# Performance work log

Hardware: AMD Instinct MI355X
Metric: run time of the kernel (lower is better)

Reference implementation:

```python
import jax, jax.numpy as jnp
import numpy as np

N = 100000       # nodes
E = 1600000      # edges (before self-loops)
IN_DIM = 64
HIDDEN = 32
HEADS = 2
OUT_DIM = 32
NEG_SLOPE = 0.2  # PyG GATConv default leaky_relu slope


def setup_inputs() -> dict:
    key = jax.random.key(0)
    ks = jax.random.split(key, 10)
    x = jax.random.normal(ks[0], (N, IN_DIM), dtype=jnp.float32)
    edge_index = jax.random.randint(ks[1], (2, E), 0, N, dtype=jnp.int64)
    s = 0.1
    W1 = jax.random.normal(ks[2], (IN_DIM, HEADS * HIDDEN), dtype=jnp.float32) * s
    a1_src = jax.random.normal(ks[3], (HEADS, HIDDEN), dtype=jnp.float32) * s
    a1_dst = jax.random.normal(ks[4], (HEADS, HIDDEN), dtype=jnp.float32) * s
    b1 = jnp.zeros((HEADS * HIDDEN,), dtype=jnp.float32)
    W2 = jax.random.normal(ks[5], (HEADS * HIDDEN, OUT_DIM), dtype=jnp.float32) * s
    a2_src = jax.random.normal(ks[6], (1, OUT_DIM), dtype=jnp.float32) * s
    a2_dst = jax.random.normal(ks[7], (1, OUT_DIM), dtype=jnp.float32) * s
    b2 = jnp.zeros((OUT_DIM,), dtype=jnp.float32)
    return {"x": x, "edge_index": edge_index,
            "W1": W1, "a1_src": a1_src, "a1_dst": a1_dst, "b1": b1,
            "W2": W2, "a2_src": a2_src, "a2_dst": a2_dst, "b2": b2}


def _gat_layer(x, src, dst, W, a_src, a_dst, bias, heads, d, concat):
    n = x.shape[0]
    # per-head linear transform: [n, heads, d]
    h = (x @ W).reshape(n, heads, d)
    # per-node attention logit halves: [n, heads]
    alpha_s = jnp.einsum('nhd,hd->nh', h, a_src)
    alpha_d = jnp.einsum('nhd,hd->nh', h, a_dst)
    # edge logits + leaky_relu: [e, heads]
    e = alpha_s[src] + alpha_d[dst]
    e = jnp.where(e >= 0, e, NEG_SLOPE * e)
    # numerically stable segment softmax over edges sharing a destination
    m = jax.ops.segment_max(e, dst, num_segments=n)          # [n, heads]
    p = jnp.exp(e - m[dst])                                  # [e, heads]
    z = jax.ops.segment_sum(p, dst, num_segments=n)          # [n, heads]
    alpha = p / z[dst]                                       # [e, heads]
    # weighted scatter-sum of source messages: [n, heads, d]
    out = jax.ops.segment_sum(alpha[:, :, None] * h[src], dst, num_segments=n)
    out = out.reshape(n, heads * d) if concat else out.mean(axis=1)
    return out + bias


def reference(x, edge_index, W1, a1_src, a1_dst, b1, W2, a2_src, a2_dst, b2):
    n = x.shape[0]
    # PyG GATConv default: add self-loops (guarantees nonempty softmax segments)
    loops = jnp.arange(n, dtype=edge_index.dtype)
    src = jnp.concatenate([edge_index[0], loops])
    dst = jnp.concatenate([edge_index[1], loops])
    h = _gat_layer(x, src, dst, W1, a1_src, a1_dst, b1, HEADS, HIDDEN, True)
    h = jax.nn.elu(h)
    # F.dropout(p=0.2) is identity at inference
    out = _gat_layer(h, src, dst, W2, a2_src, a2_dst, b2, 1, OUT_DIM, False)
    return out
```

## Files before the change

### kernel.cpp

```cpp
#include <hip/hip_runtime.h>
#include <math.h>

#define N_NODES 100000
#define E_EDGES 1600000
#define EA (E_EDGES + N_NODES)
#define NEG_SLOPE 0.2f
#define LG_BUCKET 8
#define BUCKET (1 << LG_BUCKET)
#define NB ((N_NODES + BUCKET - 1) >> LG_BUCKET)
#define LG_SLOTS 13
#define SLOTS (1 << LG_SLOTS)
#define CH 8192
#define NPB ((EA + CH - 1) / CH)
#define NLIN1 (N_NODES / 16)
#define SRC_BITS 17
#define SRC_MASK ((1u << SRC_BITS) - 1)
#define CAP 96

typedef _Float16 f16;
typedef _Float16 half2v __attribute__((ext_vector_type(2)));

__device__ __forceinline__ float leaky(float e) { return e >= 0.f ? e : NEG_SLOPE * e; }
__device__ __forceinline__ unsigned h2u(half2v h) { return __builtin_bit_cast(unsigned, h); }
__device__ __forceinline__ half2v u2h(unsigned u) { return __builtin_bit_cast(half2v, u); }
__device__ __forceinline__ half2v cvtpk(float a, float b) {
    return __builtin_bit_cast(half2v, __builtin_amdgcn_cvt_pkrtz(a, b));
}


__global__ __launch_bounds__(256) void part_lin1_kernel(
        const int* __restrict__ src, const int* __restrict__ dst,
        int* __restrict__ bcnt, unsigned* __restrict__ edges,
        const float* __restrict__ x, const float* __restrict__ W1,
        const float* __restrict__ a1s, const float* __restrict__ a1d,
        f16* __restrict__ h1, float* __restrict__ as1, float* __restrict__ ad1) {
    __shared__ int hist[NB];
    __shared__ int base[NB];
    __shared__ float Wl[64 * 64];
    __shared__ float xs[16 * 64];
    int t = threadIdx.x;
    if (blockIdx.x < NPB) {
        for (int i = t; i < NB; i += 256) hist[i] = 0;
        __syncthreads();
        int e0 = blockIdx.x * CH;
        int e1 = e0 + CH < EA ? e0 + CH : EA;
        for (int e = e0 + t; e < e1; e += 256) {
            int d = (e < E_EDGES) ? dst[e] : (e - E_EDGES);
            atomicAdd(&hist[d >> LG_BUCKET], 1);
        }
        __syncthreads();
        for (int i = t; i < NB; i += 256) {
            int h = hist[i];
            base[i] = h ? atomicAdd(&bcnt[i], h) : 0;
            hist[i] = 0;
        }
        __syncthreads();
        for (int e = e0 + t; e < e1; e += 256) {
            int s, d;
            if (e < E_EDGES) { s = src[e]; d = dst[e]; } else { s = e - E_EDGES; d = s; }
            int b = d >> LG_BUCKET;
            int r = base[b] + atomicAdd(&hist[b], 1);
            if (r < SLOTS)
                edges[(b << LG_SLOTS) + r] = ((unsigned)(d & (BUCKET - 1)) << SRC_BITS) | (unsigned)s;
        }
    } else {
        int r0 = (blockIdx.x - NPB) * 16;
        const float4* W4 = (const float4*)W1;
        float4* Wl4 = (float4*)Wl;
        #pragma unroll
        for (int i = 0; i < 4; i++) Wl4[t + i * 256] = W4[t + i * 256];
        ((float4*)xs)[t] = ((const float4*)(x + (size_t)r0 * 64))[t];
        __syncthreads();
        int c = t & 63, tg = t >> 6;
        float acc0 = 0.f, acc1 = 0.f, acc2 = 0.f, acc3 = 0.f;
        #pragma unroll
        for (int k = 0; k < 64; k++) {
            float w = Wl[k * 64 + c];
            acc0 += xs[(tg * 4 + 0) * 64 + k] * w;
            acc1 += xs[(tg * 4 + 1) * 64 + k] * w;
            acc2 += xs[(tg * 4 + 2) * 64 + k] * w;
            acc3 += xs[(tg * 4 + 3) * 64 + k] * w;
        }
        int r = r0 + tg * 4;
        h1[(size_t)(r + 0) * 64 + c] = (f16)acc0;
        h1[(size_t)(r + 1) * 64 + c] = (f16)acc1;
        h1[(size_t)(r + 2) * 64 + c] = (f16)acc2;
        h1[(size_t)(r + 3) * 64 + c] = (f16)acc3;
        float s_c = a1s[c], d_c = a1d[c];
        float vs0 = acc0 * s_c, vd0 = acc0 * d_c;
        float vs1 = acc1 * s_c, vd1 = acc1 * d_c;
        float vs2 = acc2 * s_c, vd2 = acc2 * d_c;
        float vs3 = acc3 * s_c, vd3 = acc3 * d_c;
        #pragma unroll
        for (int off = 16; off > 0; off >>= 1) {
            vs0 += __shfl_xor(vs0, off); vd0 += __shfl_xor(vd0, off);
            vs1 += __shfl_xor(vs1, off); vd1 += __shfl_xor(vd1, off);
            vs2 += __shfl_xor(vs2, off); vd2 += __shfl_xor(vd2, off);
            vs3 += __shfl_xor(vs3, off); vd3 += __shfl_xor(vd3, off);
        }
        if ((c & 31) == 0) {
            int h = c >> 5;
            as1[(r + 0) * 2 + h] = vs0; ad1[(r + 0) * 2 + h] = vd0;
            as1[(r + 1) * 2 + h] = vs1; ad1[(r + 1) * 2 + h] = vd1;
            as1[(r + 2) * 2 + h] = vs2; ad1[(r + 2) * 2 + h] = vd2;
            as1[(r + 3) * 2 + h] = vs3; ad1[(r + 3) * 2 + h] = vd3;
        }
    }
}

__global__ __launch_bounds__(256) void bucket_scatter(unsigned* __restrict__ edges,
                                                      const int* __restrict__ bcnt,
                                                      int2* __restrict__ rowSD) {
    __shared__ unsigned stage[SLOTS];
    __shared__ int hist[256];
    __shared__ int sc[256];
    int b = blockIdx.x;
    int t = threadIdx.x;
    int node0 = b << LG_BUCKET;
    int cnt = bcnt[b]; if (cnt > SLOTS) cnt = SLOTS;
    int baseg = b << LG_SLOTS;
    hist[t] = 0;
    __syncthreads();
    for (int i = t; i < cnt; i += 256) {
        unsigned p = edges[baseg + i];
        stage[i] = p;
        atomicAdd(&hist[p >> SRC_BITS], 1);
    }
    __syncthreads();
    int v = hist[t];
    sc[t] = v;
    __syncthreads();
    for (int off = 1; off < 256; off <<= 1) {
        int x = (t >= off) ? sc[t - off] : 0;
        __syncthreads();
        sc[t] += x;
        __syncthreads();
    }
    int excl = sc[t] - v;
    if (t < BUCKET && node0 + t < N_NODES) rowSD[node0 + t] = make_int2(baseg + excl, v);
    hist[t] = excl;
    __syncthreads();
    for (int i = t; i < cnt; i += 256) {
        unsigned p = stage[i];
        int r = atomicAdd(&hist[p >> SRC_BITS], 1);
        edges[baseg + r] = p & SRC_MASK;
    }
}


__global__ __launch_bounds__(256) void agg1_kernel(
        const int2* __restrict__ rowSD, const int* __restrict__ srcs,
        const f16* __restrict__ h1, const float* __restrict__ as1,
        const float* __restrict__ ad1, const float* __restrict__ b1,
        const float* __restrict__ W2, const float* __restrict__ a2s,
        const float* __restrict__ a2d,
        f16* __restrict__ h2, float* __restrict__ as2, float* __restrict__ ad2) {
    __shared__ float rowb[32][68];
    __shared__ float W2l[64 * 32];
    int tid = threadIdx.x;
    for (int i = tid; i < 2048; i += 256) W2l[i] = W2[i];
    int owid = tid >> 3;
    int l = tid & 7;
    int hh = l >> 2;
    int v = blockIdx.x * 32 + owid;
    int2 sd = rowSD[v];
    int start = sd.x, deg = sd.y;
    float2 adv = ((const float2*)ad1)[v];
    const float2* as1v2 = (const float2*)as1;
    const uint4* h1q = (const uint4*)h1;
    unsigned psel = hh ? 0x03020302u : 0x01000100u;
    half2v ax0 = {}, ax1 = {}, ax2 = {}, ax3 = {};
    half2v bx0 = {}, bx1 = {}, bx2 = {}, bx3 = {};
    float z0 = 0.f, z1 = 0.f;
    for (int c = 0; c < deg; c += 8) {
        int cnt = deg - c; if (cnt > 8) cnt = 8;
        int sreg = 0, pki = 0;
        if (c + l < deg) {
            sreg = srcs[start + c + l];
            float2 a = as1v2[sreg];
            half2v pk = cvtpk(__expf(leaky(a.x + adv.x)), __expf(leaky(a.y + adv.y)));
            z0 += (float)pk.x;
            z1 += (float)pk.y;
            pki = (int)h2u(pk);
        }
        int j = 0;
        for (; j + 1 < cnt; j += 2) {
            int s0 = __shfl(sreg, j, 8), s1 = __shfl(sreg, j + 1, 8);
            unsigned u0 = (unsigned)__shfl(pki, j, 8);
            unsigned u1 = (unsigned)__shfl(pki, j + 1, 8);
            uint4 g0 = h1q[(size_t)s0 * 8 + l];
            uint4 g1 = h1q[(size_t)s1 * 8 + l];
            half2v p0 = u2h(__builtin_amdgcn_perm(u0, u0, psel));
            half2v p1 = u2h(__builtin_amdgcn_perm(u1, u1, psel));
            ax0 += p0 * u2h(g0.x); ax1 += p0 * u2h(g0.y);
            ax2 += p0 * u2h(g0.z); ax3 += p0 * u2h(g0.w);
            bx0 += p1 * u2h(g1.x); bx1 += p1 * u2h(g1.y);
            bx2 += p1 * u2h(g1.z); bx3 += p1 * u2h(g1.w);
        }
        if (j < cnt) {
            int s0 = __shfl(sreg, j, 8);
            unsigned u0 = (unsigned)__shfl(pki, j, 8);
            uint4 g0 = h1q[(size_t)s0 * 8 + l];
            half2v p0 = u2h(__builtin_amdgcn_perm(u0, u0, psel));
            ax0 += p0 * u2h(g0.x); ax1 += p0 * u2h(g0.y);
            ax2 += p0 * u2h(g0.z); ax3 += p0 * u2h(g0.w);
        }
    }
    #pragma unroll
    for (int off = 4; off > 0; off >>= 1) {
        z0 += __shfl_xor(z0, off);
        z1 += __shfl_xor(z1, off);
    }
    float rz = 1.f / (hh ? z1 : z0);
    half2v t0 = ax0 + bx0, t1 = ax1 + bx1, t2 = ax2 + bx2, t3 = ax3 + bx3;
    float4 ba = ((const float4*)b1)[2 * l];
    float4 bb = ((const float4*)b1)[2 * l + 1];
    float o0 = (float)t0.x * rz + ba.x;
    float o1 = (float)t0.y * rz + ba.y;
    float o2 = (float)t1.x * rz + ba.z;
    float o3 = (float)t1.y * rz + ba.w;
    float o4 = (float)t2.x * rz + bb.x;
    float o5 = (float)t2.y * rz + bb.y;
    float o6 = (float)t3.x * rz + bb.z;
    float o7 = (float)t3.y * rz + bb.w;
    o0 = o0 > 0.f ? o0 : __expf(o0) - 1.f;
    o1 = o1 > 0.f ? o1 : __expf(o1) - 1.f;
    o2 = o2 > 0.f ? o2 : __expf(o2) - 1.f;
    o3 = o3 > 0.f ? o3 : __expf(o3) - 1.f;
    o4 = o4 > 0.f ? o4 : __expf(o4) - 1.f;
    o5 = o5 > 0.f ? o5 : __expf(o5) - 1.f;
    o6 = o6 > 0.f ? o6 : __expf(o6) - 1.f;
    o7 = o7 > 0.f ? o7 : __expf(o7) - 1.f;
    rowb[owid][8 * l]     = o0;
    rowb[owid][8 * l + 1] = o1;
    rowb[owid][8 * l + 2] = o2;
    rowb[owid][8 * l + 3] = o3;
    rowb[owid][8 * l + 4] = o4;
    rowb[owid][8 * l + 5] = o5;
    rowb[owid][8 * l + 6] = o6;
    rowb[owid][8 * l + 7] = o7;
    __syncthreads();
    float hc0 = 0.f, hc1 = 0.f, hc2 = 0.f, hc3 = 0.f;
    #pragma unroll 8
    for (int k = 0; k < 64; k++) {
        float r = rowb[owid][k];
        hc0 += r * W2l[k * 32 + 4 * l];
        hc1 += r * W2l[k * 32 + 4 * l + 1];
        hc2 += r * W2l[k * 32 + 4 * l + 2];
        hc3 += r * W2l[k * 32 + 4 * l + 3];
    }
    half2v hlo, hhi;
    hlo.x = (f16)hc0; hlo.y = (f16)hc1;
    hhi.x = (f16)hc2; hhi.y = (f16)hc3;
    uint2 hw; hw.x = h2u(hlo); hw.y = h2u(hhi);
    ((uint2*)h2)[(size_t)v * 8 + l] = hw;
    float4 sa = ((const float4*)a2s)[l];
    float4 da = ((const float4*)a2d)[l];
    float vs = hc0 * sa.x + hc1 * sa.y + hc2 * sa.z + hc3 * sa.w;
    float vd = hc0 * da.x + hc1 * da.y + hc2 * da.z + hc3 * da.w;
    #pragma unroll
    for (int off = 4; off > 0; off >>= 1) { vs += __shfl_xor(vs, off); vd += __shfl_xor(vd, off); }
    if (l == 0) { as2[v] = vs; ad2[v] = vd; }
}


__global__ __launch_bounds__(256) void agg2_kernel(
        const int2* __restrict__ rowSD, const int* __restrict__ srcs,
        const f16* __restrict__ h2, const float* __restrict__ as2,
        const float* __restrict__ ad2, const float* __restrict__ b2,
        float* __restrict__ out) {
    __shared__ float pbuf2[4][CAP];
    int wid = threadIdx.x >> 6;
    int v = blockIdx.x * 4 + wid;
    int lane = threadIdx.x & 63;
    int2 sd = rowSD[v];
    int start = sd.x, deg = sd.y;
    float adv = ad2[v];
    float z = 0.f;
    if (deg <= CAP) {
        for (int idx = lane; idx < deg; idx += 64) {
            int s = srcs[start + idx];
            float p = __expf(leaky(as2[s] + adv));
            pbuf2[wid][idx] = p;
            z += p;
        }
        #pragma unroll
        for (int off = 32; off > 0; off >>= 1) z += __shfl_xor(z, off);
        int q8 = lane >> 3, f8 = lane & 7;
        const uint2* h2q = (const uint2*)h2;
        float a0 = 0.f, a1 = 0.f, a2 = 0.f, a3 = 0.f;
        int idx = q8;
        for (; idx + 8 < deg; idx += 16) {
            int s0 = srcs[start + idx];
            int s1 = srcs[start + idx + 8];
            float p0 = pbuf2[wid][idx];
            float p1 = pbuf2[wid][idx + 8];
            uint2 g0 = h2q[(size_t)s0 * 8 + f8];
            uint2 g1 = h2q[(size_t)s1 * 8 + f8];
            half2v l0 = u2h(g0.x), hi0 = u2h(g0.y);
            half2v l1 = u2h(g1.x), hi1 = u2h(g1.y);
            a0 += p0 * (float)l0.x  + p1 * (float)l1.x;
            a1 += p0 * (float)l0.y  + p1 * (float)l1.y;
            a2 += p0 * (float)hi0.x + p1 * (float)hi1.x;
            a3 += p0 * (float)hi0.y + p1 * (float)hi1.y;
        }
        if (idx < deg) {
            int s0 = srcs[start + idx];
            float p0 = pbuf2[wid][idx];
            uint2 g0 = h2q[(size_t)s0 * 8 + f8];
            half2v l0 = u2h(g0.x), hi0 = u2h(g0.y);
            a0 += p0 * (float)l0.x;
            a1 += p0 * (float)l0.y;
            a2 += p0 * (float)hi0.x;
            a3 += p0 * (float)hi0.y;
        }
        #pragma unroll
        for (int off = 8; off < 64; off <<= 1) {
            a0 += __shfl_xor(a0, off);
            a1 += __shfl_xor(a1, off);
            a2 += __shfl_xor(a2, off);
            a3 += __shfl_xor(a3, off);
        }
        if (lane < 8) {
            float rz = 1.f / z;
            float4 r;
            r.x = a0 * rz + b2[4 * f8];
            r.y = a1 * rz + b2[4 * f8 + 1];
            r.z = a2 * rz + b2[4 * f8 + 2];
            r.w = a3 * rz + b2[4 * f8 + 3];
            ((float4*)out)[(size_t)v * 8 + f8] = r;
        }
    } else {
        int q = lane >> 4, f = lane & 15;
        const half2v* h2v = (const half2v*)h2;
        float a0 = 0.f, a1 = 0.f;
        float m = -1e30f;
        for (int idx = lane; idx < deg; idx += 64)
            m = fmaxf(m, leaky(as2[srcs[start + idx]] + adv));
        #pragma unroll
        for (int off = 32; off > 0; off >>= 1) m = fmaxf(m, __shfl_xor(m, off));
        for (int idx = lane; idx < deg; idx += 64)
            z += __expf(leaky(as2[srcs[start + idx]] + adv) - m);
        #pragma unroll
        for (int off = 32; off > 0; off >>= 1) z += __shfl_xor(z, off);
        for (int idx = q; idx < deg; idx += 4) {
            int s0 = srcs[start + idx];
            float p0 = __expf(leaky(as2[s0] + adv) - m);
            half2v g0 = h2v[(size_t)s0 * 16 + f];
            a0 += p0 * (float)g0.x; a1 += p0 * (float)g0.y;
        }
        a0 += __shfl_xor(a0, 16); a1 += __shfl_xor(a1, 16);
        a0 += __shfl_xor(a0, 32); a1 += __shfl_xor(a1, 32);
        if (lane < 16) {
            float rz = 1.f / z;
            float2 r;
            r.x = a0 * rz + b2[2 * f];
            r.y = a1 * rz + b2[2 * f + 1];
            ((float2*)out)[(size_t)v * 16 + f] = r;
        }
    }
}


extern "C" void kernel_launch(void* const* d_in, const int* in_sizes, int n_in,
                              void* d_out, int out_size, void* d_ws, size_t ws_size,
                              hipStream_t stream) {
    const float* x    = (const float*)d_in[0];
    const int*   ei   = (const int*)d_in[1];
    const float* W1   = (const float*)d_in[2];
    const float* a1s  = (const float*)d_in[3];
    const float* a1d  = (const float*)d_in[4];
    const float* b1   = (const float*)d_in[5];
    const float* W2   = (const float*)d_in[6];
    const float* a2s  = (const float*)d_in[7];
    const float* a2d  = (const float*)d_in[8];
    const float* b2   = (const float*)d_in[9];
    const int* src = ei;
    const int* dst = ei + E_EDGES;
    float* out = (float*)d_out;

    size_t o = 0;
    int2* rowSD     = (int2*)((int*)d_ws + o);     o += ((2 * N_NODES + 63) / 64) * 64;
    int* bcnt       = (int*)d_ws + o;              o += ((NB + 63) / 64) * 64;
    unsigned* edges = (unsigned*)((int*)d_ws + o); o += (size_t)NB * SLOTS;
    f16* h1         = (f16*)((int*)d_ws + o);      o += (size_t)N_NODES * 32;
    f16* h2         = (f16*)((int*)d_ws + o);      o += (size_t)N_NODES * 16;
    float* as1      = (float*)d_ws + o;            o += (size_t)N_NODES * 2;
    float* ad1      = (float*)d_ws + o;            o += (size_t)N_NODES * 2;
    float* as2      = (float*)d_ws + o;            o += (size_t)N_NODES;
    float* ad2      = (float*)d_ws + o;            o += (size_t)N_NODES;
    const int* srcs = (const int*)edges;

    (void)hipMemsetAsync(bcnt, 0, NB * sizeof(int), stream);
    part_lin1_kernel<<<NPB + NLIN1, 256, 0, stream>>>(src, dst, bcnt, edges,
                                                      x, W1, a1s, a1d, h1, as1, ad1);
    bucket_scatter<<<NB, 256, 0, stream>>>(edges, bcnt, rowSD);

    agg1_kernel<<<N_NODES / 32, 256, 0, stream>>>(rowSD, srcs, h1, as1, ad1, b1,
                                                  W2, a2s, a2d, h2, as2, ad2);
    agg2_kernel<<<N_NODES / 4, 256, 0, stream>>>(rowSD, srcs, h2, as2, ad2, b2, out);
}
```

Before: 153.7 us.

## Aggregate layer-2 with 4 lanes per node using packed fp16 accumulation

Restructures agg2 so each destination node is handled by a group of 4 lanes instead of a full 64-lane wavefront. Sources and softmax weights are broadcast within the group by shuffles, and the LDS buffer and large-degree max-subtraction path are dropped. Each lane loads 16-byte fp16 chunks and accumulates with packed half2 FMAs. The aim is to avoid idle lanes and cross-lane reductions at the average degree of about 17, but fp16 accumulation and skipping max-subtraction risk accuracy and overflow on high-degree nodes.

```diff
diff --git a/kernel.cpp b/kernel.cpp
--- a/kernel.cpp
+++ b/kernel.cpp
@@ -15,7 +15,6 @@
 #define NLIN1 (N_NODES / 16)
 #define SRC_BITS 17
 #define SRC_MASK ((1u << SRC_BITS) - 1)
-#define CAP 96
 
 typedef _Float16 f16;
 typedef _Float16 half2v __attribute__((ext_vector_type(2)));
@@ -269,96 +268,67 @@
         const f16* __restrict__ h2, const float* __restrict__ as2,
         const float* __restrict__ ad2, const float* __restrict__ b2,
         float* __restrict__ out) {
-    __shared__ float pbuf2[4][CAP];
-    int wid = threadIdx.x >> 6;
-    int v = blockIdx.x * 4 + wid;
-    int lane = threadIdx.x & 63;
+    int tid = threadIdx.x;
+    int owid = tid >> 2;
+    int l = tid & 3;
+    int v = blockIdx.x * 64 + owid;
+    if (v >= N_NODES) return;
     int2 sd = rowSD[v];
     int start = sd.x, deg = sd.y;
     float adv = ad2[v];
+    const uint4* h2q = (const uint4*)h2;
+    half2v ax0 = {}, ax1 = {}, ax2 = {}, ax3 = {};
+    half2v bx0 = {}, bx1 = {}, bx2 = {}, bx3 = {};
     float z = 0.f;
-    if (deg <= CAP) {
-        for (int idx = lane; idx < deg; idx += 64) {
-            int s = srcs[start + idx];
-            float p = __expf(leaky(as2[s] + adv));
-            pbuf2[wid][idx] = p;
-            z += p;
-        }
-        #pragma unroll
-        for (int off = 32; off > 0; off >>= 1) z += __shfl_xor(z, off);
-        int q8 = lane >> 3, f8 = lane & 7;
-        const uint2* h2q = (const uint2*)h2;
-        float a0 = 0.f, a1 = 0.f, a2 = 0.f, a3 = 0.f;
-        int idx = q8;
-        for (; idx + 8 < deg; idx += 16) {
-            int s0 = srcs[start + idx];
-            int s1 = srcs[start + idx + 8];
-            float p0 = pbuf2[wid][idx];
-            float p1 = pbuf2[wid][idx + 8];
-            uint2 g0 = h2q[(size_t)s0 * 8 + f8];
-            uint2 g1 = h2q[(size_t)s1 * 8 + f8];
-            half2v l0 = u2h(g0.x), hi0 = u2h(g0.y);
-            half2v l1 = u2h(g1.x), hi1 = u2h(g1.y);
-            a0 += p0 * (float)l0.x  + p1 * (float)l1.x;
-            a1 += p0 * (float)l0.y  + p1 * (float)l1.y;
-            a2 += p0 * (float)hi0.x + p1 * (float)hi1.x;
-            a3 += p0 * (float)hi0.y + p1 * (float)hi1.y;
-        }
-        if (idx < deg) {
-            int s0 = srcs[start + idx];
-            float p0 = pbuf2[wid][idx];
-            uint2 g0 = h2q[(size_t)s0 * 8 + f8];
-            half2v l0 = u2h(g0.x), hi0 = u2h(g0.y);
-            a0 += p0 * (float)l0.x;
-            a1 += p0 * (float)l0.y;
-            a2 += p0 * (float)hi0.x;
-            a3 += p0 * (float)hi0.y;
-        }
-        #pragma unroll
-        for (int off = 8; off < 64; off <<= 1) {
-            a0 += __shfl_xor(a0, off);
-            a1 += __shfl_xor(a1, off);
-            a2 += __shfl_xor(a2, off);
-            a3 += __shfl_xor(a3, off);
-        }
-        if (lane < 8) {
-            float rz = 1.f / z;
-            float4 r;
-            r.x = a0 * rz + b2[4 * f8];
-            r.y = a1 * rz + b2[4 * f8 + 1];
-            r.z = a2 * rz + b2[4 * f8 + 2];
-            r.w = a3 * rz + b2[4 * f8 + 3];
-            ((float4*)out)[(size_t)v * 8 + f8] = r;
-        }
-    } else {
-        int q = lane >> 4, f = lane & 15;
-        const half2v* h2v = (const half2v*)h2;
-        float a0 = 0.f, a1 = 0.f;
-        float m = -1e30f;
-        for (int idx = lane; idx < deg; idx += 64)
-            m = fmaxf(m, leaky(as2[srcs[start + idx]] + adv));
-        #pragma unroll
-        for (int off = 32; off > 0; off >>= 1) m = fmaxf(m, __shfl_xor(m, off));
-        for (int idx = lane; idx < deg; idx += 64)
-            z += __expf(leaky(as2[srcs[start + idx]] + adv) - m);
-        #pragma unroll
-        for (int off = 32; off > 0; off >>= 1) z += __shfl_xor(z, off);
-        for (int idx = q; idx < deg; idx += 4) {
-            int s0 = srcs[start + idx];
-            float p0 = __expf(leaky(as2[s0] + adv) - m);
-            half2v g0 = h2v[(size_t)s0 * 16 + f];
-            a0 += p0 * (float)g0.x; a1 += p0 * (float)g0.y;
-        }
-        a0 += __shfl_xor(a0, 16); a1 += __shfl_xor(a1, 16);
-        a0 += __shfl_xor(a0, 32); a1 += __shfl_xor(a1, 32);
-        if (lane < 16) {
-            float rz = 1.f / z;
-            float2 r;
-            r.x = a0 * rz + b2[2 * f];
-            r.y = a1 * rz + b2[2 * f + 1];
-            ((float2*)out)[(size_t)v * 16 + f] = r;
-        }
-    }
+    for (int c = 0; c < deg; c += 4) {
+        int cnt = deg - c; if (cnt > 4) cnt = 4;
+        int sreg = 0, pki = 0;
+        if (c + l < deg) {
+            sreg = srcs[start + c + l];
+            float p = __expf(leaky(as2[sreg] + adv));
+            half2v pk = cvtpk(p, p);
+            z += (float)pk.x;
+            pki = (int)h2u(pk);
+        }
+        int j = 0;
+        for (; j + 1 < cnt; j += 2) {
+            int s0 = __shfl(sreg, j, 4), s1 = __shfl(sreg, j + 1, 4);
+            unsigned u0 = (unsigned)__shfl(pki, j, 4);
+            unsigned u1 = (unsigned)__shfl(pki, j + 1, 4);
+            uint4 g0 = h2q[(size_t)s0 * 4 + l];
+            uint4 g1 = h2q[(size_t)s1 * 4 + l];
+            half2v p0 = u2h(u0), p1 = u2h(u1);
+            ax0 += p0 * u2h(g0.x); ax1 += p0 * u2h(g0.y);
+            ax2 += p0 * u2h(g0.z); ax3 += p0 * u2h(g0.w);
+            bx0 += p1 * u2h(g1.x); bx1 += p1 * u2h(g1.y);
+            bx2 += p1 * u2h(g1.z); bx3 += p1 * u2h(g1.w);
+        }
+        if (j < cnt) {
+            int s0 = __shfl(sreg, j, 4);
+            unsigned u0 = (unsigned)__shfl(pki, j, 4);
+            uint4 g0 = h2q[(size_t)s0 * 4 + l];
+            half2v p0 = u2h(u0);
+            ax0 += p0 * u2h(g0.x); ax1 += p0 * u2h(g0.y);
+            ax2 += p0 * u2h(g0.z); ax3 += p0 * u2h(g0.w);
+        }
+    }
+    z += __shfl_xor(z, 2);
+    z += __shfl_xor(z, 1);
+    float rz = 1.f / z;
+    half2v t0 = ax0 + bx0, t1 = ax1 + bx1, t2 = ax2 + bx2, t3 = ax3 + bx3;
+    float4 b2a = ((const float4*)b2)[2 * l];
+    float4 b2b = ((const float4*)b2)[2 * l + 1];
+    float4 r0, r1;
+    r0.x = (float)t0.x * rz + b2a.x;
+    r0.y = (float)t0.y * rz + b2a.y;
+    r0.z = (float)t1.x * rz + b2a.z;
+    r0.w = (float)t1.y * rz + b2a.w;
+    r1.x = (float)t2.x * rz + b2b.x;
+    r1.y = (float)t2.y * rz + b2b.y;
+    r1.z = (float)t3.x * rz + b2b.z;
+    r1.w = (float)t3.y * rz + b2b.w;
+    ((float4*)out)[(size_t)v * 8 + 2 * l]     = r0;
+    ((float4*)out)[(size_t)v * 8 + 2 * l + 1] = r1;
 }
 
 
@@ -398,5 +368,5 @@
 
     agg1_kernel<<<N_NODES / 32, 256, 0, stream>>>(rowSD, srcs, h1, as1, ad1, b1,
                                                   W2, a2s, a2d, h2, as2, ad2);
-    agg2_kernel<<<N_NODES / 4, 256, 0, stream>>>(rowSD, srcs, h2, as2, ad2, b2, out);
-}
+    agg2_kernel<<<(N_NODES + 63) / 64, 256, 0, stream>>>(rowSD, srcs, h2, as2, ad2, b2, out);
+}
```

New measurement: 140.4 us. -8.7%, faster.
